# Kernel tuning notes

Hardware: AMD Instinct MI355X
Metric: run time of the kernel (lower is better)

The kernel has to match this reference:

```python
import jax, jax.numpy as jnp
import numpy as np

DELTA_V = 0.5
DELTA_D = 3.0
ALPHA = 1.0
BETA = 1.0
GAMMA = 0.001
K = 5  # max instance label (labels 1..K; 0 = background)


def setup_inputs() -> dict:
    key = jax.random.key(0)
    k1, k2 = jax.random.split(key)
    B, D, H, W = 8, 8, 512, 1024
    embedding = jax.random.normal(k1, (B, D, H, W), dtype=jnp.float32)
    instance_mask = jax.random.randint(k2, (B, H, W), 0, K + 1, dtype=jnp.int32)
    return {"embedding": embedding, "instance_mask": instance_mask}


def _disc_loss(embedding, instance_mask):
    B, D, H, W = embedding.shape
    P = H * W
    emb = embedding.transpose(0, 2, 3, 1).reshape(B, P, D)      # [B,P,D]
    labels = instance_mask.reshape(B, P)                         # [B,P]

    # one-hot over instance labels 1..K (background excluded)
    onehot = (labels[..., None] == jnp.arange(1, K + 1, dtype=labels.dtype)).astype(emb.dtype)  # [B,P,K]
    counts = onehot.sum(axis=1)                                  # [B,K]
    present = counts > 0                                         # [B,K]
    presentf = present.astype(emb.dtype)
    N = presentf.sum(axis=-1)                                    # [B] num instances

    # per-instance centers via segment mean
    sums = jnp.einsum('bpd,bpk->bkd', emb, onehot)               # [B,K,D]
    centers = sums / jnp.maximum(counts, 1.0)[..., None]         # [B,K,D]

    # ---- variance loss: per-pixel distance to own center ----
    idx = jnp.clip(labels - 1, 0, K - 1)                         # [B,P]
    c_pix = jnp.take_along_axis(centers, idx[..., None], axis=1) # [B,P,D]
    d = jnp.sqrt(jnp.sum((emb - c_pix) ** 2, axis=-1))           # [B,P]
    val = jnp.maximum(d - DELTA_V, 0.0) ** 2                     # [B,P]
    inst_sum = jnp.einsum('bp,bpk->bk', val, onehot)             # [B,K]
    inst_mean = inst_sum / jnp.maximum(counts, 1.0)
    loss_var_b = (inst_mean * presentf).sum(-1) / jnp.maximum(N, 1.0)  # [B]

    # ---- distance loss: pairwise center hinge ----
    diff = centers[:, :, None, :] - centers[:, None, :, :]       # [B,K,K,D]
    dist_sq = jnp.sum(diff ** 2, axis=-1)                        # [B,K,K]
    iu = jnp.triu(jnp.ones((K, K), dtype=bool), k=1)             # i<j
    pair_mask = present[:, :, None] & present[:, None, :] & iu   # [B,K,K]
    safe_dist = jnp.sqrt(jnp.where(pair_mask, dist_sq, 1.0))
    term = jnp.maximum(2.0 * DELTA_D - safe_dist, 0.0) ** 2 * pair_mask.astype(emb.dtype)
    n_pairs = N * (N - 1.0) / 2.0
    loss_dist_b = term.sum((-1, -2)) / jnp.where(N > 1, n_pairs, 1.0)  # [B]

    # ---- regularization: mean norm of present centers ----
    c_norm = jnp.sqrt(jnp.where(present, jnp.sum(centers ** 2, axis=-1), 1.0))
    loss_reg_b = (c_norm * presentf).sum(-1) / jnp.maximum(N, 1.0)     # [B]

    # ---- batch mean over images that have at least one instance ----
    has = (N > 0).astype(emb.dtype)                              # [B]
    denom = jnp.maximum(has.sum(), 1.0)
    loss_var = (loss_var_b * has).sum() / denom
    loss_dist = (loss_dist_b * has).sum() / denom
    loss_reg = (loss_reg_b * has).sum() / denom
    total = ALPHA * loss_var + BETA * loss_dist + GAMMA * loss_reg
    return (total, loss_var, loss_dist, loss_reg)


def reference(embedding, instance_mask):
    return _disc_loss(embedding, instance_mask)
```

## Files before the change

kernel.cpp:

```cpp
#include <hip/hip_runtime.h>
#include <math.h>

constexpr int NB   = 8;
constexpr int ND   = 8;
constexpr int NH   = 512;
constexpr int NW   = 1024;
constexpr int NP   = NH * NW;
constexpr int NG   = NP / 4;
constexpr int NK   = 5;

constexpr int BPB1 = 256;
constexpr int GPB1 = NG / BPB1;
constexpr int IT1  = GPB1 / 32;
constexpr int BPB2 = 256;
constexpr int GPB2 = NG / BPB2;

constexpr float DELTA_V     = 0.5f;
constexpr float TWO_DELTA_D = 6.0f;
constexpr float GAMMA       = 0.001f;

typedef float f32x4 __attribute__((ext_vector_type(4)));
typedef int   i32x4 __attribute__((ext_vector_type(4)));

__device__ __forceinline__ float wave_sum(float v) {
#pragma unroll
    for (int off = 32; off > 0; off >>= 1) v += __shfl_down(v, off, 64);
    return v;
}

__global__ __launch_bounds__(256) void pass1_kernel(const float* __restrict__ emb,
                                                    const int* __restrict__ mask,
                                                    float* __restrict__ sums,
                                                    float* __restrict__ cnts) {
    const int b    = blockIdx.x / BPB1;
    const int blk  = blockIdx.x % BPB1;
    const int wave = threadIdx.x >> 6;
    const int lane = threadIdx.x & 63;
    const int gl   = lane & 31;
    const int d    = wave * 2 + (lane >> 5);
    const bool dzero = (d == 0);

    const f32x4* __restrict__ ep = (const f32x4*)emb + (long)(b * ND + d) * NG;
    const int4*  __restrict__ mp = (const int4*)mask + (long)b * NG;

    float a0 = 0.f, a1 = 0.f, a2 = 0.f, a3 = 0.f, a4 = 0.f;
    float n0 = 0.f, n1 = 0.f, n2 = 0.f, n3 = 0.f, n4 = 0.f;

    const int base = blk * GPB1 + gl;

#define PIX1(LAB, EJ) { const int lab = (LAB); const float ej = (EJ); \
        a0 += (lab == 1) ? ej : 0.f; a1 += (lab == 2) ? ej : 0.f; \
        a2 += (lab == 3) ? ej : 0.f; a3 += (lab == 4) ? ej : 0.f; \
        a4 += (lab == 5) ? ej : 0.f; \
        if (dzero) { n0 += (lab == 1) ? 1.f : 0.f; n1 += (lab == 2) ? 1.f : 0.f; \
                     n2 += (lab == 3) ? 1.f : 0.f; n3 += (lab == 4) ? 1.f : 0.f; \
                     n4 += (lab == 5) ? 1.f : 0.f; } }

#pragma unroll
    for (int it = 0; it < IT1; it += 2) {
        const int ga = base + it * 32;
        const int gb = ga + 32;
        const int4  ma = mp[ga];
        const f32x4 ea = __builtin_nontemporal_load(ep + ga);
        const int4  mb = mp[gb];
        const f32x4 eb = __builtin_nontemporal_load(ep + gb);
        PIX1(ma.x, ea.x) PIX1(ma.y, ea.y) PIX1(ma.z, ea.z) PIX1(ma.w, ea.w)
        PIX1(mb.x, eb.x) PIX1(mb.y, eb.y) PIX1(mb.z, eb.z) PIX1(mb.w, eb.w)
    }
#undef PIX1

#pragma unroll
    for (int off = 16; off > 0; off >>= 1) {
        a0 += __shfl_down(a0, off, 32); a1 += __shfl_down(a1, off, 32);
        a2 += __shfl_down(a2, off, 32); a3 += __shfl_down(a3, off, 32);
        a4 += __shfl_down(a4, off, 32);
    }
    if (wave == 0) {
#pragma unroll
        for (int off = 16; off > 0; off >>= 1) {
            n0 += __shfl_down(n0, off, 32); n1 += __shfl_down(n1, off, 32);
            n2 += __shfl_down(n2, off, 32); n3 += __shfl_down(n3, off, 32);
            n4 += __shfl_down(n4, off, 32);
        }
    }

    __shared__ float pl[ND][NK];
    __shared__ float pc[NK];
    if (gl == 0) {
        pl[d][0] = a0; pl[d][1] = a1; pl[d][2] = a2; pl[d][3] = a3; pl[d][4] = a4;
    }
    if (threadIdx.x == 0) { pc[0] = n0; pc[1] = n1; pc[2] = n2; pc[3] = n3; pc[4] = n4; }
    __syncthreads();
    const int t = threadIdx.x;
    if (t < NK * ND)
        atomicAdd(&sums[b * NK * ND + t], pl[t & 7][t >> 3]);
    else if (t < NK * ND + NK)
        atomicAdd(&cnts[b * NK + (t - NK * ND)], pc[t - NK * ND]);
}

__global__ __launch_bounds__(256) void pass2_kernel(const float* __restrict__ emb,
                                                    const int* __restrict__ mask,
                                                    const float* __restrict__ sums,
                                                    const float* __restrict__ cnts,
                                                    float* __restrict__ vsums) {
    const int b   = blockIdx.x / BPB2;
    const int blk = blockIdx.x % BPB2;
    const long base = (long)blk * GPB2;

    const float* sp = sums + b * NK * ND;
    const float i0 = 1.f / fmaxf(cnts[b * NK + 0], 1.f);
    const float i1 = 1.f / fmaxf(cnts[b * NK + 1], 1.f);
    const float i2 = 1.f / fmaxf(cnts[b * NK + 2], 1.f);
    const float i3 = 1.f / fmaxf(cnts[b * NK + 3], 1.f);
    const float i4 = 1.f / fmaxf(cnts[b * NK + 4], 1.f);
    const float4 c0l = make_float4(sp[0]*i0,  sp[1]*i0,  sp[2]*i0,  sp[3]*i0);
    const float4 c0h = make_float4(sp[4]*i0,  sp[5]*i0,  sp[6]*i0,  sp[7]*i0);
    const float4 c1l = make_float4(sp[8]*i1,  sp[9]*i1,  sp[10]*i1, sp[11]*i1);
    const float4 c1h = make_float4(sp[12]*i1, sp[13]*i1, sp[14]*i1, sp[15]*i1);
    const float4 c2l = make_float4(sp[16]*i2, sp[17]*i2, sp[18]*i2, sp[19]*i2);
    const float4 c2h = make_float4(sp[20]*i2, sp[21]*i2, sp[22]*i2, sp[23]*i2);
    const float4 c3l = make_float4(sp[24]*i3, sp[25]*i3, sp[26]*i3, sp[27]*i3);
    const float4 c3h = make_float4(sp[28]*i3, sp[29]*i3, sp[30]*i3, sp[31]*i3);
    const float4 c4l = make_float4(sp[32]*i4, sp[33]*i4, sp[34]*i4, sp[35]*i4);
    const float4 c4h = make_float4(sp[36]*i4, sp[37]*i4, sp[38]*i4, sp[39]*i4);

    const f32x4* __restrict__ emb4 = (const f32x4*)emb + (long)b * ND * NG;
    const i32x4* __restrict__ m4p  = (const i32x4*)mask + (long)b * NG;

    float v0 = 0.f, v1 = 0.f, v2 = 0.f, v3 = 0.f, v4 = 0.f;

    for (int it = threadIdx.x; it < GPB2; it += 256) {
        const long g = base + it;
        const i32x4 m  = __builtin_nontemporal_load(m4p + g);
        const f32x4 e0 = __builtin_nontemporal_load(emb4 + g);
        const f32x4 e1 = __builtin_nontemporal_load(emb4 + g + (long)NG);
        const f32x4 e2 = __builtin_nontemporal_load(emb4 + g + 2L * NG);
        const f32x4 e3 = __builtin_nontemporal_load(emb4 + g + 3L * NG);
        const f32x4 e4 = __builtin_nontemporal_load(emb4 + g + 4L * NG);
        const f32x4 e5 = __builtin_nontemporal_load(emb4 + g + 5L * NG);
        const f32x4 e6 = __builtin_nontemporal_load(emb4 + g + 6L * NG);
        const f32x4 e7 = __builtin_nontemporal_load(emb4 + g + 7L * NG);

#define SEL2(F) ((lab == 1) ? c0##F : (lab == 2) ? c1##F : (lab == 3) ? c2##F : \
                 (lab == 4) ? c3##F : c4##F)
#define PIX2(LAB, CM) { const int lab = (LAB); \
        float dd = e0.CM - SEL2(l.x); float dsq = dd * dd; \
        dd = e1.CM - SEL2(l.y); dsq = fmaf(dd, dd, dsq); \
        dd = e2.CM - SEL2(l.z); dsq = fmaf(dd, dd, dsq); \
        dd = e3.CM - SEL2(l.w); dsq = fmaf(dd, dd, dsq); \
        dd = e4.CM - SEL2(h.x); dsq = fmaf(dd, dd, dsq); \
        dd = e5.CM - SEL2(h.y); dsq = fmaf(dd, dd, dsq); \
        dd = e6.CM - SEL2(h.z); dsq = fmaf(dd, dd, dsq); \
        dd = e7.CM - SEL2(h.w); dsq = fmaf(dd, dd, dsq); \
        const float dist = sqrtf(dsq); \
        const float hv = fmaxf(dist - DELTA_V, 0.f); \
        const float val = hv * hv; \
        v0 += (lab == 1) ? val : 0.f; v1 += (lab == 2) ? val : 0.f; \
        v2 += (lab == 3) ? val : 0.f; v3 += (lab == 4) ? val : 0.f; \
        v4 += (lab == 5) ? val : 0.f; }

        PIX2(m.x, x) PIX2(m.y, y) PIX2(m.z, z) PIX2(m.w, w)
#undef PIX2
#undef SEL2
    }

    __shared__ float part[4][NK];
    const int lane = threadIdx.x & 63;
    const int wave = threadIdx.x >> 6;
#define RED2(V, IDX) { const float r = wave_sum(V); if (lane == 0) part[wave][IDX] = r; }
    RED2(v0, 0) RED2(v1, 1) RED2(v2, 2) RED2(v3, 3) RED2(v4, 4)
#undef RED2
    __syncthreads();
    if (threadIdx.x < NK) {
        const float s = part[0][threadIdx.x] + part[1][threadIdx.x] +
                        part[2][threadIdx.x] + part[3][threadIdx.x];
        atomicAdd(&vsums[b * NK + threadIdx.x], s);
    }
}

__global__ void final_kernel(const float* __restrict__ sums,
                             const float* __restrict__ cnts,
                             const float* __restrict__ vsums,
                             float* __restrict__ out) {
    __shared__ float bl[4][NB];
    const int bb = threadIdx.x;
    if (bb < NB) {
        float cc[NK];
        bool  pres[NK];
        float c[NK][ND];
        float N = 0.f;
#pragma unroll
        for (int k = 0; k < NK; ++k) {
            cc[k]   = cnts[bb * NK + k];
            pres[k] = cc[k] > 0.f;
            if (pres[k]) N += 1.f;
            const float inv = 1.f / fmaxf(cc[k], 1.f);
#pragma unroll
            for (int d = 0; d < ND; ++d)
                c[k][d] = sums[bb * NK * ND + k * ND + d] * inv;
        }
        float lv = 0.f;
#pragma unroll
        for (int k = 0; k < NK; ++k)
            if (pres[k]) lv += vsums[bb * NK + k] / fmaxf(cc[k], 1.f);
        lv /= fmaxf(N, 1.f);
        float ld = 0.f;
#pragma unroll
        for (int i = 0; i < NK; ++i)
#pragma unroll
            for (int j = i + 1; j < NK; ++j)
                if (pres[i] && pres[j]) {
                    float dsq = 0.f;
#pragma unroll
                    for (int d = 0; d < ND; ++d) {
                        const float df = c[i][d] - c[j][d];
                        dsq = fmaf(df, df, dsq);
                    }
                    const float t = fmaxf(TWO_DELTA_D - sqrtf(dsq), 0.f);
                    ld += t * t;
                }
        const float npairs = N * (N - 1.f) * 0.5f;
        ld /= (N > 1.f) ? npairs : 1.f;
        float lr = 0.f;
#pragma unroll
        for (int k = 0; k < NK; ++k)
            if (pres[k]) {
                float sq = 0.f;
#pragma unroll
                for (int d = 0; d < ND; ++d) sq = fmaf(c[k][d], c[k][d], sq);
                lr += sqrtf(sq);
            }
        lr /= fmaxf(N, 1.f);

        const float has = (N > 0.f) ? 1.f : 0.f;
        bl[0][bb] = lv * has;
        bl[1][bb] = ld * has;
        bl[2][bb] = lr * has;
        bl[3][bb] = has;
    }
    __syncthreads();
    if (threadIdx.x == 0) {
        float tv = 0.f, td = 0.f, tr = 0.f, hs = 0.f;
        for (int i = 0; i < NB; ++i) {
            tv += bl[0][i]; td += bl[1][i]; tr += bl[2][i]; hs += bl[3][i];
        }
        const float denom = fmaxf(hs, 1.f);
        tv /= denom; td /= denom; tr /= denom;
        out[0] = tv + td + GAMMA * tr;
        out[1] = tv;
        out[2] = td;
        out[3] = tr;
    }
}

extern "C" void kernel_launch(void* const* d_in, const int* in_sizes, int n_in,
                              void* d_out, int out_size, void* d_ws, size_t ws_size,
                              hipStream_t stream) {
    const float* emb  = (const float*)d_in[0];
    const int*   mask = (const int*)d_in[1];
    float* out = (float*)d_out;

    float* sums  = (float*)d_ws;
    float* cnts  = sums + NB * NK * ND;
    float* vsums = cnts + NB * NK;

    hipMemsetAsync(d_ws, 0, (size_t)(NB * NK * ND + 2 * NB * NK) * sizeof(float), stream);

    pass1_kernel<<<dim3(NB * BPB1), dim3(256), 0, stream>>>(emb, mask, sums, cnts);
    pass2_kernel<<<dim3(NB * BPB2), dim3(256), 0, stream>>>(emb, mask, sums, cnts, vsums);
    final_kernel<<<1, 64, 0, stream>>>(sums, cnts, vsums, out);
}
```

Baseline: 256.5 us.

## Restructure pass1 so each thread loads mask once and loops over channels

Pass 1 previously gave each half-wave one embedding channel, so every channel group re-read the mask. Now each thread reads its mask pixels once, counts labels, then walks all 8 channels with a one-step software prefetch of the next channel's embedding values. Per-channel partial sums go through full-wave reductions into shared memory and are combined across the four waves before the atomics. This cuts redundant mask traffic and computes the counts once. In exchange the per-channel loop is serialized with unroll 1 and needs more shuffle reductions, which may reduce memory-level parallelism.

```diff
diff --git a/kernel.cpp b/kernel.cpp
--- a/kernel.cpp
+++ b/kernel.cpp
@@ -11,7 +11,6 @@
 
 constexpr int BPB1 = 256;
 constexpr int GPB1 = NG / BPB1;
-constexpr int IT1  = GPB1 / 32;
 constexpr int BPB2 = 256;
 constexpr int GPB2 = NG / BPB2;
 
@@ -34,68 +33,71 @@
                                                     float* __restrict__ cnts) {
     const int b    = blockIdx.x / BPB1;
     const int blk  = blockIdx.x % BPB1;
-    const int wave = threadIdx.x >> 6;
-    const int lane = threadIdx.x & 63;
-    const int gl   = lane & 31;
-    const int d    = wave * 2 + (lane >> 5);
-    const bool dzero = (d == 0);
-
-    const f32x4* __restrict__ ep = (const f32x4*)emb + (long)(b * ND + d) * NG;
-    const int4*  __restrict__ mp = (const int4*)mask + (long)b * NG;
-
-    float a0 = 0.f, a1 = 0.f, a2 = 0.f, a3 = 0.f, a4 = 0.f;
+    const int t    = threadIdx.x;
+    const int lane = t & 63;
+    const int wave = t >> 6;
+
+    __shared__ float psum[4][ND][NK];
+    __shared__ float pcnt[4][NK];
+
+    const int4*   __restrict__ mp = (const int4*)mask + (long)b * NG + blk * GPB1;
+    const float4* __restrict__ ep = (const float4*)emb + (long)b * ND * NG + blk * GPB1;
+
+    const int4 m0 = mp[t];
+    const int4 m1 = mp[t + 256];
+
     float n0 = 0.f, n1 = 0.f, n2 = 0.f, n3 = 0.f, n4 = 0.f;
-
-    const int base = blk * GPB1 + gl;
-
-#define PIX1(LAB, EJ) { const int lab = (LAB); const float ej = (EJ); \
-        a0 += (lab == 1) ? ej : 0.f; a1 += (lab == 2) ? ej : 0.f; \
-        a2 += (lab == 3) ? ej : 0.f; a3 += (lab == 4) ? ej : 0.f; \
-        a4 += (lab == 5) ? ej : 0.f; \
-        if (dzero) { n0 += (lab == 1) ? 1.f : 0.f; n1 += (lab == 2) ? 1.f : 0.f; \
-                     n2 += (lab == 3) ? 1.f : 0.f; n3 += (lab == 4) ? 1.f : 0.f; \
-                     n4 += (lab == 5) ? 1.f : 0.f; } }
-
-#pragma unroll
-    for (int it = 0; it < IT1; it += 2) {
-        const int ga = base + it * 32;
-        const int gb = ga + 32;
-        const int4  ma = mp[ga];
-        const f32x4 ea = __builtin_nontemporal_load(ep + ga);
-        const int4  mb = mp[gb];
-        const f32x4 eb = __builtin_nontemporal_load(ep + gb);
-        PIX1(ma.x, ea.x) PIX1(ma.y, ea.y) PIX1(ma.z, ea.z) PIX1(ma.w, ea.w)
-        PIX1(mb.x, eb.x) PIX1(mb.y, eb.y) PIX1(mb.z, eb.z) PIX1(mb.w, eb.w)
-    }
-#undef PIX1
-
-#pragma unroll
-    for (int off = 16; off > 0; off >>= 1) {
-        a0 += __shfl_down(a0, off, 32); a1 += __shfl_down(a1, off, 32);
-        a2 += __shfl_down(a2, off, 32); a3 += __shfl_down(a3, off, 32);
-        a4 += __shfl_down(a4, off, 32);
-    }
-    if (wave == 0) {
-#pragma unroll
-        for (int off = 16; off > 0; off >>= 1) {
-            n0 += __shfl_down(n0, off, 32); n1 += __shfl_down(n1, off, 32);
-            n2 += __shfl_down(n2, off, 32); n3 += __shfl_down(n3, off, 32);
-            n4 += __shfl_down(n4, off, 32);
-        }
-    }
-
-    __shared__ float pl[ND][NK];
-    __shared__ float pc[NK];
-    if (gl == 0) {
-        pl[d][0] = a0; pl[d][1] = a1; pl[d][2] = a2; pl[d][3] = a3; pl[d][4] = a4;
-    }
-    if (threadIdx.x == 0) { pc[0] = n0; pc[1] = n1; pc[2] = n2; pc[3] = n3; pc[4] = n4; }
+#define CNT1(L) { const int lb = (L); \
+        n0 += (lb == 1) ? 1.f : 0.f; n1 += (lb == 2) ? 1.f : 0.f; \
+        n2 += (lb == 3) ? 1.f : 0.f; n3 += (lb == 4) ? 1.f : 0.f; \
+        n4 += (lb == 5) ? 1.f : 0.f; }
+    CNT1(m0.x) CNT1(m0.y) CNT1(m0.z) CNT1(m0.w)
+    CNT1(m1.x) CNT1(m1.y) CNT1(m1.z) CNT1(m1.w)
+#undef CNT1
+    n0 = wave_sum(n0); n1 = wave_sum(n1); n2 = wave_sum(n2);
+    n3 = wave_sum(n3); n4 = wave_sum(n4);
+    if (lane == 0) {
+        pcnt[wave][0] = n0; pcnt[wave][1] = n1; pcnt[wave][2] = n2;
+        pcnt[wave][3] = n3; pcnt[wave][4] = n4;
+    }
+
+    float4 ex = ep[t];
+    float4 ey = ep[t + 256];
+#pragma unroll 1
+    for (int d = 0; d < ND; ++d) {
+        const float4 cx = ex;
+        const float4 cy = ey;
+        if (d < ND - 1) {
+            ex = ep[(long)(d + 1) * NG + t];
+            ey = ep[(long)(d + 1) * NG + t + 256];
+        }
+        float a0 = 0.f, a1 = 0.f, a2 = 0.f, a3 = 0.f, a4 = 0.f;
+#define ACC1(EV, LB) { const int lb = (LB); const float e = (EV); \
+        a0 += (lb == 1) ? e : 0.f; a1 += (lb == 2) ? e : 0.f; \
+        a2 += (lb == 3) ? e : 0.f; a3 += (lb == 4) ? e : 0.f; \
+        a4 += (lb == 5) ? e : 0.f; }
+        ACC1(cx.x, m0.x) ACC1(cx.y, m0.y) ACC1(cx.z, m0.z) ACC1(cx.w, m0.w)
+        ACC1(cy.x, m1.x) ACC1(cy.y, m1.y) ACC1(cy.z, m1.z) ACC1(cy.w, m1.w)
+#undef ACC1
+        a0 = wave_sum(a0); a1 = wave_sum(a1); a2 = wave_sum(a2);
+        a3 = wave_sum(a3); a4 = wave_sum(a4);
+        if (lane == 0) {
+            psum[wave][d][0] = a0; psum[wave][d][1] = a1; psum[wave][d][2] = a2;
+            psum[wave][d][3] = a3; psum[wave][d][4] = a4;
+        }
+    }
     __syncthreads();
-    const int t = threadIdx.x;
-    if (t < NK * ND)
-        atomicAdd(&sums[b * NK * ND + t], pl[t & 7][t >> 3]);
-    else if (t < NK * ND + NK)
-        atomicAdd(&cnts[b * NK + (t - NK * ND)], pc[t - NK * ND]);
+
+    if (t < NK * ND) {
+        const int k = t >> 3, d = t & 7;
+        const float s = psum[0][d][k] + psum[1][d][k] +
+                        psum[2][d][k] + psum[3][d][k];
+        atomicAdd(&sums[b * NK * ND + t], s);
+    } else if (t < NK * ND + NK) {
+        const int k = t - NK * ND;
+        atomicAdd(&cnts[b * NK + k],
+                  pcnt[0][k] + pcnt[1][k] + pcnt[2][k] + pcnt[3][k]);
+    }
 }
 
 __global__ __launch_bounds__(256) void pass2_kernel(const float* __restrict__ emb,
```

New measurement: 255.4 us. Within noise of the previous version (-0.4%).
